# Performance work log

Hardware: AMD Instinct MI355X
Metric: run time of the kernel (lower is better)

The kernel has to match this reference:

```python
import jax, jax.numpy as jnp
import numpy as np

H = 64  # latent_dim // 2


def _lstm_cell(x, h, c, Wih, Whh, b):
    # PyTorch gate order: i, f, g, o
    g = x @ Wih.T + h @ Whh.T + b
    i, f, gg, o = jnp.split(g, 4, axis=-1)
    c = jax.nn.sigmoid(f) * c + jax.nn.sigmoid(i) * jnp.tanh(gg)
    h = jax.nn.sigmoid(o) * jnp.tanh(c)
    return h, c


def _run_lstm(x, Wih, Whh, b):
    # x: [B, T, D] -> outputs [B, T, H], final h, c (zero-initialized state)
    B = x.shape[0]
    h0 = jnp.zeros((B, Whh.shape[1]), x.dtype)

    def step(carry, xt):
        h, c = _lstm_cell(xt, carry[0], carry[1], Wih, Whh, b)
        return (h, c), h

    (h, c), ys = jax.lax.scan(step, (h0, h0), jnp.swapaxes(x, 0, 1))
    return jnp.swapaxes(ys, 0, 1), h, c


def setup_inputs() -> dict:
    key = jax.random.key(0)
    ks = jax.random.split(key, 16)
    B, S, T, D = 512, 1024, 512, 3
    s = 1.0 / np.sqrt(H)

    def u(k, shape):
        return jax.random.uniform(k, shape, jnp.float32, -s, s)

    return {
        "src": jax.random.normal(ks[0], (B, S, D), jnp.float32),
        "trg": jax.random.normal(ks[1], (B, T, D), jnp.float32),
        "enc1_Wih": u(ks[2], (4 * H, D)),
        "enc1_Whh": u(ks[3], (4 * H, H)),
        "enc1_b": u(ks[4], (4 * H,)),
        "enc2_Wih": u(ks[5], (4 * H, H)),
        "enc2_Whh": u(ks[6], (4 * H, H)),
        "enc2_b": u(ks[7], (4 * H,)),
        "dec1_Wih": u(ks[8], (4 * H, D)),
        "dec1_Whh": u(ks[9], (4 * H, H)),
        "dec1_b": u(ks[10], (4 * H,)),
        "dec2_Wih": u(ks[11], (4 * H, H)),
        "dec2_Whh": u(ks[12], (4 * H, H)),
        "dec2_b": u(ks[13], (4 * H,)),
        "fc_W": u(ks[14], (D, H)),
        "fc_b": u(ks[15], (D,)),
    }


def reference(src, trg, enc1_Wih, enc1_Whh, enc1_b, enc2_Wih, enc2_Whh, enc2_b,
              dec1_Wih, dec1_Whh, dec1_b, dec2_Wih, dec2_Whh, dec2_b, fc_W, fc_b):
    # Encoder: two stacked LSTMs over src; keep final state of layer 2.
    y1, _, _ = _run_lstm(src, enc1_Wih, enc1_Whh, enc1_b)
    _, h, c = _run_lstm(y1, enc2_Wih, enc2_Whh, enc2_b)

    # Decoder (teacher_forcing_ratio = 1.0, the only well-defined branch):
    # at each step both decoder LSTMs share/chain the SAME (h, c) state,
    # exactly as the original Decoder.forward does with seq-len-1 inputs.
    def step(carry, xt):
        h, c = carry
        h1, c1 = _lstm_cell(xt, h, c, dec1_Wih, dec1_Whh, dec1_b)
        h2, c2 = _lstm_cell(h1, h1, c1, dec2_Wih, dec2_Whh, dec2_b)
        return (h2, c2), h2 @ fc_W.T + fc_b

    xs = jnp.swapaxes(trg[:, :-1, :], 0, 1)  # inputs for t = 1..T-1
    _, preds = jax.lax.scan(step, (h, c), xs)
    preds = jnp.swapaxes(preds, 0, 1)  # [B, T-1, 3]

    B = trg.shape[0]
    zero0 = jnp.zeros((B, 1, fc_b.shape[0]), preds.dtype)  # outputs[:, 0] stays 0
    return jnp.concatenate([zero0, preds], axis=1)
```

## Files before the change

### kernel.cpp

```cpp
#include <hip/hip_runtime.h>
#include <math.h>

typedef _Float16 f16;
typedef _Float16 f16x8 __attribute__((ext_vector_type(8)));
typedef float    f32x4 __attribute__((ext_vector_type(4)));

#define MFMA16(A, B, C) __builtin_amdgcn_mfma_f32_16x16x32_f16((A), (B), (C), 0, 0, 0)
#define LOG2E 1.44269504088896f

__device__ __forceinline__ float sig2(float a) {
    return __builtin_amdgcn_rcpf(1.0f + __builtin_amdgcn_exp2f(a));
}
__device__ __forceinline__ float tanh2(float c) {
    return fmaf(2.0f, sig2(c * (-2.0f * LOG2E)), -1.0f);
}

__device__ __forceinline__ f16x8 ldfrag(const float* __restrict__ W, int n, int k0, float s) {
    const float* p = W + (size_t)n * 64 + k0;
    f16x8 r;
#pragma unroll
    for (int j = 0; j < 8; j++) r[j] = (f16)(s * p[j]);
    return r;
}

__global__ __launch_bounds__(512, 2)
void seq2seq_kernel(const float* __restrict__ src, const float* __restrict__ trg,
                    const float* __restrict__ e1ih, const float* __restrict__ e1hh,
                    const float* __restrict__ e1b,
                    const float* __restrict__ e2ih, const float* __restrict__ e2hh,
                    const float* __restrict__ e2b,
                    const float* __restrict__ d1ih, const float* __restrict__ d1hh,
                    const float* __restrict__ d1b,
                    const float* __restrict__ d2ih, const float* __restrict__ d2hh,
                    const float* __restrict__ d2b,
                    const float* __restrict__ fcW, const float* __restrict__ fcb,
                    float* __restrict__ out)
{
    const int bp   = blockIdx.x;
    const int tid  = threadIdx.x;
    const int wv   = tid >> 6;
    const bool isB = (wv >= 4);
    const int wvg  = wv & 3;
    const int lane = tid & 63;
    const int quad = lane >> 4;
    const int c15  = lane & 15;
    const int u16  = wvg * 16 + c15;
    const int qb   = quad & 1;
    const int ab   = c15 & 1;

    __shared__ __align__(16) float xst[1024][8];
    __shared__ __align__(16) float tst[512][8];
    __shared__ __align__(16) f16 h1l[2][2][64];
    __shared__ __align__(16) f16 h2l[2][2][64];
    __shared__ float c1buf[2][64];
    __shared__ float c2buf[2][64];
    __shared__ __align__(16) f16 ring[2][16][72];

    {
        const float* s0 = src + (size_t)(2 * bp) * 3072;
        const float* s1 = s0 + 3072;
        for (int i = tid; i < 3072; i += 512) {
            int t = i / 3, c = i - 3 * t;
            xst[t][c]     = s0[i];
            xst[t][4 + c] = s1[i];
        }
        const float* t0p = trg + (size_t)(2 * bp) * 1536;
        const float* t1p = t0p + 1536;
        for (int i = tid; i < 1536; i += 512) {
            int t = i / 3, c = i - 3 * t;
            tst[t][c]     = t0p[i];
            tst[t][4 + c] = t1p[i];
        }
    }

    f16x8 E1hh[4][2];
    f16x8 E2ih[4][2], E2hh[4][2];
    float xw[4][3], bias1[4];
    f32x4 bs2[4];
    if (!isB) {
#pragma unroll
        for (int g = 0; g < 4; g++) {
            const float s = (g == 2) ? (-2.0f * LOG2E) : (-LOG2E);
            const int n = g * 64 + u16;
#pragma unroll
            for (int c = 0; c < 2; c++)
                E1hh[g][c] = ldfrag(e1hh, n, c * 32 + quad * 8, s);
            xw[g][0] = s * e1ih[n * 3 + 0];
            xw[g][1] = s * e1ih[n * 3 + 1];
            xw[g][2] = s * e1ih[n * 3 + 2];
            bias1[g] = s * e1b[n];
        }
    } else {
#pragma unroll
        for (int g = 0; g < 4; g++) {
            const float s = (g == 2) ? (-2.0f * LOG2E) : (-LOG2E);
            const int n = g * 64 + u16;
#pragma unroll
            for (int c = 0; c < 2; c++) {
                E2ih[g][c] = ldfrag(e2ih, n, c * 32 + quad * 8, s);
                E2hh[g][c] = ldfrag(e2hh, n, c * 32 + quad * 8, s);
            }
            float bv = s * e2b[n];
            bs2[g] = (f32x4){bv, bv, bv, bv};
        }
    }

    float c1 = 0.f, c2 = 0.f;
    if (tid < 256) {
        (&h1l[0][0][0])[tid] = (f16)0.f;
        (&h2l[0][0][0])[tid] = (f16)0.f;
    }
    __syncthreads();

    const f32x4 z4 = {0.f, 0.f, 0.f, 0.f};

    f32x4 xq = z4, xnq = z4;
    if (!isB) xq = *(const f32x4*)&xst[0][qb * 4];

#pragma unroll 1
    for (int tau = 0; tau <= 1024; tau++) {
        const int w = tau & 1;
        if (!isB) {
            if (tau < 1024) {
                const f16* h1p = h1l[w ^ 1][ab];
                f16x8 a0 = *(const f16x8*)(h1p + quad * 8);
                f16x8 a1 = *(const f16x8*)(h1p + 32 + quad * 8);
                float xt[4];
#pragma unroll
                for (int g = 0; g < 4; g++)
                    xt[g] = fmaf(xw[g][0], xq.x,
                            fmaf(xw[g][1], xq.y, fmaf(xw[g][2], xq.z, bias1[g])));
                f32x4 acc[4];
#pragma unroll
                for (int g = 0; g < 4; g++)
                    acc[g] = MFMA16(a1, E1hh[g][1], MFMA16(a0, E1hh[g][0], z4));
                float v[4];
#pragma unroll
                for (int g = 0; g < 4; g++)
                    v[g] = (qb ? acc[g][1] : acc[g][0]) + xt[g];
                float iv = sig2(v[0]), fv = sig2(v[1]);
                float gv = fmaf(2.0f, sig2(v[2]), -1.0f), ov = sig2(v[3]);
                c1 = fv * c1 + iv * gv;
                if (quad < 2) h1l[w][quad][u16] = (f16)(ov * tanh2(c1));
                const int tn = (tau + 1 < 1024) ? tau + 1 : 1023;
                xnq = *(const f32x4*)&xst[tn][qb * 4];
            }
        } else {
            if (tau > 0) {
                const f16* h1p = h1l[w ^ 1][ab];
                const f16* h2p = h2l[w ^ 1][ab];
                f16x8 a0 = *(const f16x8*)(h1p + quad * 8);
                f16x8 a1 = *(const f16x8*)(h1p + 32 + quad * 8);
                f16x8 b0 = *(const f16x8*)(h2p + quad * 8);
                f16x8 b1 = *(const f16x8*)(h2p + 32 + quad * 8);
                f32x4 accA[4], accB[4];
#pragma unroll
                for (int g = 0; g < 4; g++) {
                    accA[g] = MFMA16(a1, E2ih[g][1], MFMA16(a0, E2ih[g][0], bs2[g]));
                    accB[g] = MFMA16(b1, E2hh[g][1], MFMA16(b0, E2hh[g][0], z4));
                }
                float v[4];
#pragma unroll
                for (int g = 0; g < 4; g++)
                    v[g] = (qb ? accA[g][1] : accA[g][0]) +
                           (qb ? accB[g][1] : accB[g][0]);
                float iv = sig2(v[0]), fv = sig2(v[1]);
                float gv = fmaf(2.0f, sig2(v[2]), -1.0f), ov = sig2(v[3]);
                c2 = fv * c2 + iv * gv;
                if (quad < 2) h2l[w][quad][u16] = (f16)(ov * tanh2(c2));
            }
        }
        __syncthreads();
        if (!isB) xq = xnq;
    }

    f16x8 D1hh[4][2];
    f16x8 W2s[4][2];
    float dxw[4][3], db1[4];
    f32x4 db2s[4];
    if (!isB) {
#pragma unroll
        for (int g = 0; g < 4; g++) {
            const float s = (g == 2) ? (-2.0f * LOG2E) : (-LOG2E);
            const int n = g * 64 + u16;
#pragma unroll
            for (int c = 0; c < 2; c++)
                D1hh[g][c] = ldfrag(d1hh, n, c * 32 + quad * 8, s);
            dxw[g][0] = s * d1ih[n * 3 + 0];
            dxw[g][1] = s * d1ih[n * 3 + 1];
            dxw[g][2] = s * d1ih[n * 3 + 2];
            db1[g] = s * d1b[n];
        }
    } else {
#pragma unroll
        for (int g = 0; g < 4; g++) {
            const float s = (g == 2) ? (-2.0f * LOG2E) : (-LOG2E);
            const int n = g * 64 + u16;
#pragma unroll
            for (int c = 0; c < 2; c++) {
                const int k0 = c * 32 + quad * 8;
                const float* pa = d2ih + (size_t)n * 64 + k0;
                const float* pb = d2hh + (size_t)n * 64 + k0;
                f16x8 r;
#pragma unroll
                for (int j = 0; j < 8; j++) r[j] = (f16)(s * (pa[j] + pb[j]));
                W2s[g][c] = r;
            }
            float bv = s * d2b[n];
            db2s[g] = (f32x4){bv, bv, bv, bv};
        }
        if (quad < 2) c2buf[quad][u16] = c2;
    }
    f16x8 FW0 = {}, FW1 = {};
    float fb = 0.f;
    if (wv >= 6 && c15 < 3) {
#pragma unroll
        for (int j = 0; j < 8; j++) {
            FW0[j] = (f16)fcW[c15 * 64 + quad * 8 + j];
            FW1[j] = (f16)fcW[c15 * 64 + 32 + quad * 8 + j];
        }
        fb = fcb[c15];
    }
    __syncthreads();

    f32x4 tq = z4, tnq = z4;
    if (!isB) tq = *(const f32x4*)&tst[0][qb * 4];

#pragma unroll 1
    for (int t = 0; t < 511; t++) {
        const int r = t & 1, w = r ^ 1;
        if (!isB) {
            const f16* hp = h2l[r][ab];
            f16x8 a0 = *(const f16x8*)(hp + quad * 8);
            f16x8 a1 = *(const f16x8*)(hp + 32 + quad * 8);
            float cdin = c2buf[qb][u16];
            float xt[4];
#pragma unroll
            for (int g = 0; g < 4; g++)
                xt[g] = fmaf(dxw[g][0], tq.x,
                        fmaf(dxw[g][1], tq.y, fmaf(dxw[g][2], tq.z, db1[g])));
            f32x4 acc[4];
#pragma unroll
            for (int g = 0; g < 4; g++)
                acc[g] = MFMA16(a1, D1hh[g][1], MFMA16(a0, D1hh[g][0], z4));
            float v[4];
#pragma unroll
            for (int g = 0; g < 4; g++)
                v[g] = (qb ? acc[g][1] : acc[g][0]) + xt[g];
            float iv = sig2(v[0]), fv = sig2(v[1]);
            float gv = fmaf(2.0f, sig2(v[2]), -1.0f), ov = sig2(v[3]);
            float c1d = fv * cdin + iv * gv;
            if (quad < 2) {
                h1l[w][quad][u16] = (f16)(ov * tanh2(c1d));
                c1buf[quad][u16]  = c1d;
            }
            const int tn = (t + 1 < 511) ? t + 1 : 510;
            tnq = *(const f32x4*)&tst[tn][qb * 4];
        } else if (wv >= 6 && t > 0 && (t & 15) == 0) {
            const int bsel = wv - 6;
            const f16* rp = &ring[bsel][0][0];
            f16x8 fa0 = *(const f16x8*)(rp + c15 * 72 + quad * 8);
            f16x8 fa1 = *(const f16x8*)(rp + c15 * 72 + 32 + quad * 8);
            f32x4 acc = MFMA16(fa1, FW1, MFMA16(fa0, FW0, z4));
            if (c15 < 3) {
                float* ob = out + (((size_t)(2 * bp + bsel) * 512 + (t - 15)) * 3) + c15;
#pragma unroll
                for (int rg = 0; rg < 4; rg++)
                    ob[(quad * 4 + rg) * 3] = acc[rg] + fb;
            }
        }
        __syncthreads();
        if (!isB) tq = tnq;

        if (isB) {
            const f16* np = h1l[w][ab];
            f16x8 m0 = *(const f16x8*)(np + quad * 8);
            f16x8 m1 = *(const f16x8*)(np + 32 + quad * 8);
            float c1in = c1buf[qb][u16];
            f32x4 acc[4];
#pragma unroll
            for (int g = 0; g < 4; g++)
                acc[g] = MFMA16(m1, W2s[g][1], MFMA16(m0, W2s[g][0], db2s[g]));
            float v[4];
#pragma unroll
            for (int g = 0; g < 4; g++)
                v[g] = (qb ? acc[g][1] : acc[g][0]);
            float i2 = sig2(v[0]), f2 = sig2(v[1]);
            float g2 = fmaf(2.0f, sig2(v[2]), -1.0f), o2 = sig2(v[3]);
            float c2d = f2 * c1in + i2 * g2;
            if (quad < 2) {
                f16 hh = (f16)(o2 * tanh2(c2d));
                h2l[w][quad][u16] = hh;
                c2buf[quad][u16]  = c2d;
                ring[quad][t & 15][u16] = hh;
            }
        }
        __syncthreads();
    }

    if (wv >= 6) {
        const int bsel = wv - 6;
        const f16* rp = &ring[bsel][0][0];
        f16x8 fa0 = *(const f16x8*)(rp + c15 * 72 + quad * 8);
        f16x8 fa1 = *(const f16x8*)(rp + c15 * 72 + 32 + quad * 8);
        f32x4 acc = MFMA16(fa1, FW1, MFMA16(fa0, FW0, z4));
        if (c15 < 3) {
            float* ob = out + (((size_t)(2 * bp + bsel) * 512 + 497) * 3) + c15;
#pragma unroll
            for (int rg = 0; rg < 4; rg++) {
                int step = quad * 4 + rg;
                if (step < 15) ob[step * 3] = acc[rg] + fb;
            }
        }
    }
}

extern "C" void kernel_launch(void* const* d_in, const int* in_sizes, int n_in,
                              void* d_out, int out_size, void* d_ws, size_t ws_size,
                              hipStream_t stream)
{
    const float* src   = (const float*)d_in[0];
    const float* trg   = (const float*)d_in[1];
    const float* e1ih  = (const float*)d_in[2];
    const float* e1hh  = (const float*)d_in[3];
    const float* e1b   = (const float*)d_in[4];
    const float* e2ih  = (const float*)d_in[5];
    const float* e2hh  = (const float*)d_in[6];
    const float* e2b   = (const float*)d_in[7];
    const float* dd1ih = (const float*)d_in[8];
    const float* dd1hh = (const float*)d_in[9];
    const float* dd1b  = (const float*)d_in[10];
    const float* dd2ih = (const float*)d_in[11];
    const float* dd2hh = (const float*)d_in[12];
    const float* dd2b  = (const float*)d_in[13];
    const float* fcW   = (const float*)d_in[14];
    const float* fcb   = (const float*)d_in[15];
    float* out = (float*)d_out;

    hipMemsetAsync(d_out, 0, (size_t)out_size * sizeof(float), stream);

    seq2seq_kernel<<<256, 512, 0, stream>>>(src, trg,
                                            e1ih, e1hh, e1b, e2ih, e2hh, e2b,
                                            dd1ih, dd1hh, dd1b, dd2ih, dd2hh, dd2b,
                                            fcW, fcb, out);
}
```

Baseline: 832.3 us.

## Split encoder LSTM step into two barrier phases so MFMA overlaps activations

```diff
diff --git a/kernel.cpp b/kernel.cpp
--- a/kernel.cpp
+++ b/kernel.cpp
@@ -114,64 +114,84 @@
 
     const f32x4 z4 = {0.f, 0.f, 0.f, 0.f};
 
-    f32x4 xq = z4, xnq = z4;
+    f32x4 xq = z4;
     if (!isB) xq = *(const f32x4*)&xst[0][qb * 4];
+
+    f32x4 accA[4], accB[4];
 
 #pragma unroll 1
     for (int tau = 0; tau <= 1024; tau++) {
-        const int w = tau & 1;
+        const int w = tau & 1, r = w ^ 1;
+
         if (!isB) {
             if (tau < 1024) {
-                const f16* h1p = h1l[w ^ 1][ab];
+                const f16* h1p = h1l[r][ab];
                 f16x8 a0 = *(const f16x8*)(h1p + quad * 8);
                 f16x8 a1 = *(const f16x8*)(h1p + 32 + quad * 8);
+                __builtin_amdgcn_s_setprio(1);
+#pragma unroll
+                for (int g = 0; g < 4; g++)
+                    accA[g] = MFMA16(a1, E1hh[g][1], MFMA16(a0, E1hh[g][0], z4));
+                __builtin_amdgcn_s_setprio(0);
+            }
+        } else if (tau >= 2) {
+            float v[4];
+#pragma unroll
+            for (int g = 0; g < 4; g++)
+                v[g] = (qb ? accA[g][1] : accA[g][0]) +
+                       (qb ? accB[g][1] : accB[g][0]);
+            float iv = sig2(v[0]), fv = sig2(v[1]);
+            float gv = fmaf(2.0f, sig2(v[2]), -1.0f), ov = sig2(v[3]);
+            c2 = fv * c2 + iv * gv;
+            if (quad < 2) h2l[w][quad][u16] = (f16)(ov * tanh2(c2));
+        }
+        __syncthreads();
+
+        if (!isB) {
+            if (tau < 1024) {
                 float xt[4];
 #pragma unroll
                 for (int g = 0; g < 4; g++)
                     xt[g] = fmaf(xw[g][0], xq.x,
                             fmaf(xw[g][1], xq.y, fmaf(xw[g][2], xq.z, bias1[g])));
-                f32x4 acc[4];
+                float v[4];
 #pragma unroll
                 for (int g = 0; g < 4; g++)
-                    acc[g] = MFMA16(a1, E1hh[g][1], MFMA16(a0, E1hh[g][0], z4));
-                float v[4];
-#pragma unroll
-                for (int g = 0; g < 4; g++)
-                    v[g] = (qb ? acc[g][1] : acc[g][0]) + xt[g];
+                    v[g] = (qb ? accA[g][1] : accA[g][0]) + xt[g];
                 float iv = sig2(v[0]), fv = sig2(v[1]);
                 float gv = fmaf(2.0f, sig2(v[2]), -1.0f), ov = sig2(v[3]);
                 c1 = fv * c1 + iv * gv;
                 if (quad < 2) h1l[w][quad][u16] = (f16)(ov * tanh2(c1));
                 const int tn = (tau + 1 < 1024) ? tau + 1 : 1023;
-                xnq = *(const f32x4*)&xst[tn][qb * 4];
-            }
-        } else {
-            if (tau > 0) {
-                const f16* h1p = h1l[w ^ 1][ab];
-                const f16* h2p = h2l[w ^ 1][ab];
-                f16x8 a0 = *(const f16x8*)(h1p + quad * 8);
-                f16x8 a1 = *(const f16x8*)(h1p + 32 + quad * 8);
-                f16x8 b0 = *(const f16x8*)(h2p + quad * 8);
-                f16x8 b1 = *(const f16x8*)(h2p + 32 + quad * 8);
-                f32x4 accA[4], accB[4];
-#pragma unroll
-                for (int g = 0; g < 4; g++) {
-                    accA[g] = MFMA16(a1, E2ih[g][1], MFMA16(a0, E2ih[g][0], bs2[g]));
-                    accB[g] = MFMA16(b1, E2hh[g][1], MFMA16(b0, E2hh[g][0], z4));
-                }
-                float v[4];
-#pragma unroll
-                for (int g = 0; g < 4; g++)
-                    v[g] = (qb ? accA[g][1] : accA[g][0]) +
-                           (qb ? accB[g][1] : accB[g][0]);
-                float iv = sig2(v[0]), fv = sig2(v[1]);
-                float gv = fmaf(2.0f, sig2(v[2]), -1.0f), ov = sig2(v[3]);
-                c2 = fv * c2 + iv * gv;
-                if (quad < 2) h2l[w][quad][u16] = (f16)(ov * tanh2(c2));
-            }
+                xq = *(const f32x4*)&xst[tn][qb * 4];
+            }
+        } else if (tau >= 1) {
+            const f16* h1p = h1l[r][ab];
+            const f16* h2p = h2l[w][ab];
+            f16x8 a0 = *(const f16x8*)(h1p + quad * 8);
+            f16x8 a1 = *(const f16x8*)(h1p + 32 + quad * 8);
+            f16x8 b0 = *(const f16x8*)(h2p + quad * 8);
+            f16x8 b1 = *(const f16x8*)(h2p + 32 + quad * 8);
+            __builtin_amdgcn_s_setprio(1);
+#pragma unroll
+            for (int g = 0; g < 4; g++) {
+                accA[g] = MFMA16(a1, E2ih[g][1], MFMA16(a0, E2ih[g][0], bs2[g]));
+                accB[g] = MFMA16(b1, E2hh[g][1], MFMA16(b0, E2hh[g][0], z4));
+            }
+            __builtin_amdgcn_s_setprio(0);
         }
         __syncthreads();
-        if (!isB) xq = xnq;
+    }
+    if (isB) {
+        float v[4];
+#pragma unroll
+        for (int g = 0; g < 4; g++)
+            v[g] = (qb ? accA[g][1] : accA[g][0]) +
+                   (qb ? accB[g][1] : accB[g][0]);
+        float iv = sig2(v[0]), fv = sig2(v[1]);
+        float gv = fmaf(2.0f, sig2(v[2]), -1.0f), ov = sig2(v[3]);
+        c2 = fv * c2 + iv * gv;
+        if (quad < 2) h2l[0][quad][u16] = (f16)(ov * tanh2(c2));
     }
 
     f16x8 D1hh[4][2];
@@ -201,10 +221,10 @@
                 const int k0 = c * 32 + quad * 8;
                 const float* pa = d2ih + (size_t)n * 64 + k0;
                 const float* pb = d2hh + (size_t)n * 64 + k0;
-                f16x8 r;
-#pragma unroll
-                for (int j = 0; j < 8; j++) r[j] = (f16)(s * (pa[j] + pb[j]));
-                W2s[g][c] = r;
+                f16x8 r2;
+#pragma unroll
+                for (int j = 0; j < 8; j++) r2[j] = (f16)(s * (pa[j] + pb[j]));
+                W2s[g][c] = r2;
             }
             float bv = s * d2b[n];
             db2s[g] = (f32x4){bv, bv, bv, bv};
@@ -240,9 +260,11 @@
                 xt[g] = fmaf(dxw[g][0], tq.x,
                         fmaf(dxw[g][1], tq.y, fmaf(dxw[g][2], tq.z, db1[g])));
             f32x4 acc[4];
+            __builtin_amdgcn_s_setprio(1);
 #pragma unroll
             for (int g = 0; g < 4; g++)
                 acc[g] = MFMA16(a1, D1hh[g][1], MFMA16(a0, D1hh[g][0], z4));
+            __builtin_amdgcn_s_setprio(0);
             float v[4];
 #pragma unroll
             for (int g = 0; g < 4; g++)
@@ -278,9 +300,11 @@
             f16x8 m1 = *(const f16x8*)(np + 32 + quad * 8);
             float c1in = c1buf[qb][u16];
             f32x4 acc[4];
+            __builtin_amdgcn_s_setprio(1);
 #pragma unroll
             for (int g = 0; g < 4; g++)
                 acc[g] = MFMA16(m1, W2s[g][1], MFMA16(m0, W2s[g][0], db2s[g]));
+            __builtin_amdgcn_s_setprio(0);
             float v[4];
 #pragma unroll
             for (int g = 0; g < 4; g++)
```

Result: slower. 1.580 ms (+89.9%).

## Replace per-step block barriers with LDS flag handshakes between wave groups

Applied to the files above, without the earlier changes.

```diff
diff --git a/kernel.cpp b/kernel.cpp
--- a/kernel.cpp
+++ b/kernel.cpp
@@ -21,6 +21,31 @@
 #pragma unroll
     for (int j = 0; j < 8; j++) r[j] = (f16)(s * p[j]);
     return r;
+}
+
+__device__ __forceinline__ void poll4(volatile unsigned* f, unsigned want) {
+    int g = 0;
+    for (;;) {
+        unsigned a = f[0], b = f[1], c = f[2], d = f[3];
+        if ((a >= want) & (b >= want) & (c >= want) & (d >= want)) break;
+        if (++g > (1 << 22)) break;
+    }
+    asm volatile("" ::: "memory");
+}
+__device__ __forceinline__ void poll44(volatile unsigned* f, unsigned wa, unsigned wb) {
+    int g = 0;
+    for (;;) {
+        unsigned a = f[0], b = f[1], c = f[2], d = f[3];
+        unsigned e = f[4], h = f[5], i = f[6], j = f[7];
+        if ((a >= wa) & (b >= wa) & (c >= wa) & (d >= wa) &
+            (e >= wb) & (h >= wb) & (i >= wb) & (j >= wb)) break;
+        if (++g > (1 << 22)) break;
+    }
+    asm volatile("" ::: "memory");
+}
+__device__ __forceinline__ void publish(volatile unsigned* f, int idx, unsigned v, bool doit) {
+    asm volatile("s_waitcnt lgkmcnt(0)" ::: "memory");
+    if (doit) f[idx] = v;
 }
 
 __global__ __launch_bounds__(512, 2)
@@ -50,11 +75,14 @@
 
     __shared__ __align__(16) float xst[1024][8];
     __shared__ __align__(16) float tst[512][8];
-    __shared__ __align__(16) f16 h1l[2][2][64];
-    __shared__ __align__(16) f16 h2l[2][2][64];
+    __shared__ __align__(16) f16 h1l[4][2][64];
+    __shared__ __align__(16) f16 h2l[4][2][64];
     __shared__ float c1buf[2][64];
     __shared__ float c2buf[2][64];
     __shared__ __align__(16) f16 ring[2][16][72];
+    __shared__ unsigned flg[16];
+
+    volatile unsigned* vflg = flg;
 
     {
         const float* s0 = src + (size_t)(2 * bp) * 3072;
@@ -106,78 +134,77 @@
     }
 
     float c1 = 0.f, c2 = 0.f;
-    if (tid < 256) {
+    if (tid < 512) {
         (&h1l[0][0][0])[tid] = (f16)0.f;
         (&h2l[0][0][0])[tid] = (f16)0.f;
     }
+    if (tid < 16) flg[tid] = 0;
     __syncthreads();
 
     const f32x4 z4 = {0.f, 0.f, 0.f, 0.f};
 
-    f32x4 xq = z4, xnq = z4;
-    if (!isB) xq = *(const f32x4*)&xst[0][qb * 4];
-
+    if (!isB) {
 #pragma unroll 1
-    for (int tau = 0; tau <= 1024; tau++) {
-        const int w = tau & 1;
-        if (!isB) {
-            if (tau < 1024) {
-                const f16* h1p = h1l[w ^ 1][ab];
-                f16x8 a0 = *(const f16x8*)(h1p + quad * 8);
-                f16x8 a1 = *(const f16x8*)(h1p + 32 + quad * 8);
-                float xt[4];
-#pragma unroll
-                for (int g = 0; g < 4; g++)
-                    xt[g] = fmaf(xw[g][0], xq.x,
-                            fmaf(xw[g][1], xq.y, fmaf(xw[g][2], xq.z, bias1[g])));
-                f32x4 acc[4];
-#pragma unroll
-                for (int g = 0; g < 4; g++)
-                    acc[g] = MFMA16(a1, E1hh[g][1], MFMA16(a0, E1hh[g][0], z4));
-                float v[4];
-#pragma unroll
-                for (int g = 0; g < 4; g++)
-                    v[g] = (qb ? acc[g][1] : acc[g][0]) + xt[g];
-                float iv = sig2(v[0]), fv = sig2(v[1]);
-                float gv = fmaf(2.0f, sig2(v[2]), -1.0f), ov = sig2(v[3]);
-                c1 = fv * c1 + iv * gv;
-                if (quad < 2) h1l[w][quad][u16] = (f16)(ov * tanh2(c1));
-                const int tn = (tau + 1 < 1024) ? tau + 1 : 1023;
-                xnq = *(const f32x4*)&xst[tn][qb * 4];
-            }
-        } else {
-            if (tau > 0) {
-                const f16* h1p = h1l[w ^ 1][ab];
-                const f16* h2p = h2l[w ^ 1][ab];
-                f16x8 a0 = *(const f16x8*)(h1p + quad * 8);
-                f16x8 a1 = *(const f16x8*)(h1p + 32 + quad * 8);
-                f16x8 b0 = *(const f16x8*)(h2p + quad * 8);
-                f16x8 b1 = *(const f16x8*)(h2p + 32 + quad * 8);
-                f32x4 accA[4], accB[4];
-#pragma unroll
-                for (int g = 0; g < 4; g++) {
-                    accA[g] = MFMA16(a1, E2ih[g][1], MFMA16(a0, E2ih[g][0], bs2[g]));
-                    accB[g] = MFMA16(b1, E2hh[g][1], MFMA16(b0, E2hh[g][0], z4));
-                }
-                float v[4];
-#pragma unroll
-                for (int g = 0; g < 4; g++)
-                    v[g] = (qb ? accA[g][1] : accA[g][0]) +
-                           (qb ? accB[g][1] : accB[g][0]);
-                float iv = sig2(v[0]), fv = sig2(v[1]);
-                float gv = fmaf(2.0f, sig2(v[2]), -1.0f), ov = sig2(v[3]);
-                c2 = fv * c2 + iv * gv;
-                if (quad < 2) h2l[w][quad][u16] = (f16)(ov * tanh2(c2));
-            }
-        }
-        __syncthreads();
-        if (!isB) xq = xnq;
+        for (unsigned tau = 0; tau < 1024; tau++) {
+            f32x4 xq = *(const f32x4*)&xst[tau][qb * 4];
+            poll44(vflg, tau, tau >= 3 ? tau - 3 : 0);
+            const f16* h1p = h1l[(tau + 3) & 3][ab];
+            f16x8 a0 = *(const f16x8*)(h1p + quad * 8);
+            f16x8 a1 = *(const f16x8*)(h1p + 32 + quad * 8);
+            float xt[4];
+#pragma unroll
+            for (int g = 0; g < 4; g++)
+                xt[g] = fmaf(xw[g][0], xq.x,
+                        fmaf(xw[g][1], xq.y, fmaf(xw[g][2], xq.z, bias1[g])));
+            f32x4 acc[4];
+#pragma unroll
+            for (int g = 0; g < 4; g++)
+                acc[g] = MFMA16(a1, E1hh[g][1], MFMA16(a0, E1hh[g][0], z4));
+            float v[4];
+#pragma unroll
+            for (int g = 0; g < 4; g++)
+                v[g] = (qb ? acc[g][1] : acc[g][0]) + xt[g];
+            float iv = sig2(v[0]), fv = sig2(v[1]);
+            float gv = fmaf(2.0f, sig2(v[2]), -1.0f), ov = sig2(v[3]);
+            c1 = fv * c1 + iv * gv;
+            if (quad < 2) h1l[tau & 3][quad][u16] = (f16)(ov * tanh2(c1));
+            publish(vflg, wvg, tau + 1, lane == 0);
+        }
+    } else {
+#pragma unroll 1
+        for (unsigned tau = 1; tau <= 1024; tau++) {
+            poll44(vflg, tau, tau - 1);
+            const f16* h1p = h1l[(tau + 3) & 3][ab];
+            const f16* h2p = h2l[(tau + 2) & 3][ab];
+            f16x8 a0 = *(const f16x8*)(h1p + quad * 8);
+            f16x8 a1 = *(const f16x8*)(h1p + 32 + quad * 8);
+            f16x8 b0 = *(const f16x8*)(h2p + quad * 8);
+            f16x8 b1 = *(const f16x8*)(h2p + 32 + quad * 8);
+            f32x4 accA[4], accB[4];
+#pragma unroll
+            for (int g = 0; g < 4; g++) {
+                accA[g] = MFMA16(a1, E2ih[g][1], MFMA16(a0, E2ih[g][0], bs2[g]));
+                accB[g] = MFMA16(b1, E2hh[g][1], MFMA16(b0, E2hh[g][0], z4));
+            }
+            float v[4];
+#pragma unroll
+            for (int g = 0; g < 4; g++)
+                v[g] = (qb ? accA[g][1] : accA[g][0]) +
+                       (qb ? accB[g][1] : accB[g][0]);
+            float iv = sig2(v[0]), fv = sig2(v[1]);
+            float gv = fmaf(2.0f, sig2(v[2]), -1.0f), ov = sig2(v[3]);
+            c2 = fv * c2 + iv * gv;
+            if (quad < 2) h2l[(tau + 3) & 3][quad][u16] = (f16)(ov * tanh2(c2));
+            publish(vflg + 4, wvg, tau, lane == 0);
+        }
     }
 
     f16x8 D1hh[4][2];
     f16x8 W2s[4][2];
     float dxw[4][3], db1[4];
     f32x4 db2s[4];
+    f16x8 FW0 = {}, FW1 = {};
+    float fb = 0.f;
     if (!isB) {
 #pragma unroll
         for (int g = 0; g < 4; g++) {
@@ -201,36 +228,32 @@
                 const int k0 = c * 32 + quad * 8;
                 const float* pa = d2ih + (size_t)n * 64 + k0;
                 const float* pb = d2hh + (size_t)n * 64 + k0;
-                f16x8 r;
-#pragma unroll
-                for (int j = 0; j < 8; j++) r[j] = (f16)(s * (pa[j] + pb[j]));
-                W2s[g][c] = r;
+                f16x8 r2;
+#pragma unroll
+                for (int j = 0; j < 8; j++) r2[j] = (f16)(s * (pa[j] + pb[j]));
+                W2s[g][c] = r2;
             }
             float bv = s * d2b[n];
             db2s[g] = (f32x4){bv, bv, bv, bv};
         }
         if (quad < 2) c2buf[quad][u16] = c2;
-    }
-    f16x8 FW0 = {}, FW1 = {};
-    float fb = 0.f;
-    if (wv >= 6 && c15 < 3) {
-#pragma unroll
-        for (int j = 0; j < 8; j++) {
-            FW0[j] = (f16)fcW[c15 * 64 + quad * 8 + j];
-            FW1[j] = (f16)fcW[c15 * 64 + 32 + quad * 8 + j];
-        }
-        fb = fcb[c15];
+        if (wv >= 6 && c15 < 3) {
+#pragma unroll
+            for (int j = 0; j < 8; j++) {
+                FW0[j] = (f16)fcW[c15 * 64 + quad * 8 + j];
+                FW1[j] = (f16)fcW[c15 * 64 + 32 + quad * 8 + j];
+            }
+            fb = fcb[c15];
+        }
     }
     __syncthreads();
 
-    f32x4 tq = z4, tnq = z4;
-    if (!isB) tq = *(const f32x4*)&tst[0][qb * 4];
-
+    if (!isB) {
 #pragma unroll 1
-    for (int t = 0; t < 511; t++) {
-        const int r = t & 1, w = r ^ 1;
-        if (!isB) {
-            const f16* hp = h2l[r][ab];
+        for (unsigned t = 0; t < 511; t++) {
+            f32x4 tq = *(const f32x4*)&tst[t][qb * 4];
+            poll4(vflg + 12, t);
+            const f16* hp = h2l[(t + 3) & 3][ab];
             f16x8 a0 = *(const f16x8*)(hp + quad * 8);
             f16x8 a1 = *(const f16x8*)(hp + 32 + quad * 8);
             float cdin = c2buf[qb][u16];
@@ -251,65 +274,66 @@
             float gv = fmaf(2.0f, sig2(v[2]), -1.0f), ov = sig2(v[3]);
             float c1d = fv * cdin + iv * gv;
             if (quad < 2) {
-                h1l[w][quad][u16] = (f16)(ov * tanh2(c1d));
+                h1l[t & 3][quad][u16] = (f16)(ov * tanh2(c1d));
                 c1buf[quad][u16]  = c1d;
             }
-            const int tn = (t + 1 < 511) ? t + 1 : 510;
-            tnq = *(const f32x4*)&tst[tn][qb * 4];
-        } else if (wv >= 6 && t > 0 && (t & 15) == 0) {
+            publish(vflg + 8, wvg, t + 1, lane == 0);
+        }
+    } else {
+#pragma unroll 1
+        for (unsigned t = 0; t < 511; t++) {
+            if (wv >= 6 && t > 0 && (t & 15) == 0) {
+                poll4(vflg + 12, t);
+                const int bsel = wv - 6;
+                const f16* rp = &ring[bsel][0][0];
+                f16x8 fa0 = *(const f16x8*)(rp + c15 * 72 + quad * 8);
+                f16x8 fa1 = *(const f16x8*)(rp + c15 * 72 + 32 + quad * 8);
+                f32x4 acc = MFMA16(fa1, FW1, MFMA16(fa0, FW0, z4));
+                if (c15 < 3) {
+                    float* ob = out + (((size_t)(2 * bp + bsel) * 512 + (t - 15)) * 3) + c15;
+#pragma unroll
+                    for (int rg = 0; rg < 4; rg++)
+                        ob[(quad * 4 + rg) * 3] = acc[rg] + fb;
+                }
+            }
+            poll4(vflg + 8, t + 1);
+            const f16* np = h1l[t & 3][ab];
+            f16x8 m0 = *(const f16x8*)(np + quad * 8);
+            f16x8 m1 = *(const f16x8*)(np + 32 + quad * 8);
+            float c1in = c1buf[qb][u16];
+            f32x4 acc[4];
+#pragma unroll
+            for (int g = 0; g < 4; g++)
+                acc[g] = MFMA16(m1, W2s[g][1], MFMA16(m0, W2s[g][0], db2s[g]));
+            float v[4];
+#pragma unroll
+            for (int g = 0; g < 4; g++)
+                v[g] = (qb ? acc[g][1] : acc[g][0]);
+            float i2 = sig2(v[0]), f2 = sig2(v[1]);
+            float g2 = fmaf(2.0f, sig2(v[2]), -1.0f), o2 = sig2(v[3]);
+            float c2d = f2 * c1in + i2 * g2;
+            if (quad < 2) {
+                f16 hh = (f16)(o2 * tanh2(c2d));
+                h2l[t & 3][quad][u16] = hh;
+                c2buf[quad][u16]  = c2d;
+                ring[quad][t & 15][u16] = hh;
+            }
+            publish(vflg + 12, wvg, t + 1, lane == 0);
+        }
+        if (wv >= 6) {
+            poll4(vflg + 12, 511);
             const int bsel = wv - 6;
             const f16* rp = &ring[bsel][0][0];
             f16x8 fa0 = *(const f16x8*)(rp + c15 * 72 + quad * 8);
             f16x8 fa1 = *(const f16x8*)(rp + c15 * 72 + 32 + quad * 8);
             f32x4 acc = MFMA16(fa1, FW1, MFMA16(fa0, FW0, z4));
             if (c15 < 3) {
-                float* ob = out + (((size_t)(2 * bp + bsel) * 512 + (t - 15)) * 3) + c15;
-#pragma unroll
-                for (int rg = 0; rg < 4; rg++)
-                    ob[(quad * 4 + rg) * 3] = acc[rg] + fb;
-            }
-        }
-        __syncthreads();
-        if (!isB) tq = tnq;
-
-        if (isB) {
-            const f16* np = h1l[w][ab];
-            f16x8 m0 = *(const f16x8*)(np + quad * 8);
-            f16x8 m1 = *(const f16x8*)(np + 32 + quad * 8);
-            float c1in = c1buf[qb][u16];
-            f32x4 acc[4];
-#pragma unroll
-            for (int g = 0; g < 4; g++)
-                acc[g] = MFMA16(m1, W2s[g][1], MFMA16(m0, W2s[g][0], db2s[g]));
-            float v[4];
-#pragma unroll
-            for (int g = 0; g < 4; g++)
-                v[g] = (qb ? acc[g][1] : acc[g][0]);
-            float i2 = sig2(v[0]), f2 = sig2(v[1]);
-            float g2 = fmaf(2.0f, sig2(v[2]), -1.0f), o2 = sig2(v[3]);
-            float c2d = f2 * c1in + i2 * g2;
-            if (quad < 2) {
-                f16 hh = (f16)(o2 * tanh2(c2d));
-                h2l[w][quad][u16] = hh;
-                c2buf[quad][u16]  = c2d;
-                ring[quad][t & 15][u16] = hh;
-            }
-        }
-        __syncthreads();
-    }
-
-    if (wv >= 6) {
-        const int bsel = wv - 6;
-        const f16* rp = &ring[bsel][0][0];
-        f16x8 fa0 = *(const f16x8*)(rp + c15 * 72 + quad * 8);
-        f16x8 fa1 = *(const f16x8*)(rp + c15 * 72 + 32 + quad * 8);
-        f32x4 acc = MFMA16(fa1, FW1, MFMA16(fa0, FW0, z4));
-        if (c15 < 3) {
-            float* ob = out + (((size_t)(2 * bp + bsel) * 512 + 497) * 3) + c15;
-#pragma unroll
-            for (int rg = 0; rg < 4; rg++) {
-                int step = quad * 4 + rg;
-                if (step < 15) ob[step * 3] = acc[rg] + fb;
+                float* ob = out + (((size_t)(2 * bp + bsel) * 512 + 497) * 3) + c15;
+#pragma unroll
+                for (int rg = 0; rg < 4; rg++) {
+                    int step = quad * 4 + rg;
+                    if (step < 15) ob[step * 3] = acc[rg] + fb;
+                }
             }
         }
     }
```

Measured after the change: 1.296 ms. 55.7% more time.

## Pipeline LSTM layers across single wavefronts with LDS flag handoff

Applied to the files above, without the earlier changes.

```diff
diff --git a/kernel.cpp b/kernel.cpp
--- a/kernel.cpp
+++ b/kernel.cpp
@@ -23,7 +23,13 @@
     return r;
 }
 
-__global__ __launch_bounds__(512, 2)
+__device__ __forceinline__ void pollge(volatile unsigned* f, unsigned want) {
+    int g = 0;
+    while (*f < want) { if (++g > (1 << 23)) break; }
+    asm volatile("" ::: "memory");
+}
+
+__global__ __launch_bounds__(256, 1)
 void seq2seq_kernel(const float* __restrict__ src, const float* __restrict__ trg,
                     const float* __restrict__ e1ih, const float* __restrict__ e1hh,
                     const float* __restrict__ e1b,
@@ -39,277 +45,307 @@
     const int bp   = blockIdx.x;
     const int tid  = threadIdx.x;
     const int wv   = tid >> 6;
-    const bool isB = (wv >= 4);
-    const int wvg  = wv & 3;
     const int lane = tid & 63;
     const int quad = lane >> 4;
     const int c15  = lane & 15;
-    const int u16  = wvg * 16 + c15;
     const int qb   = quad & 1;
     const int ab   = c15 & 1;
 
-    __shared__ __align__(16) float xst[1024][8];
-    __shared__ __align__(16) float tst[512][8];
-    __shared__ __align__(16) f16 h1l[2][2][64];
-    __shared__ __align__(16) f16 h2l[2][2][64];
-    __shared__ float c1buf[2][64];
+    __shared__ __align__(16) f16 xst[1024][8];
+    __shared__ __align__(16) f16 tst[512][8];
+    __shared__ __align__(16) f16 h1r[16][2][64];
+    __shared__ __align__(16) f16 h2b[2][64];
+    __shared__ __align__(16) f16 h1d[2][64];
     __shared__ float c2buf[2][64];
-    __shared__ __align__(16) f16 ring[2][16][72];
+    __shared__ __align__(16) f16 ring[2][32][72];
+    __shared__ unsigned flg[4];
+    volatile unsigned* vflg = flg;
 
     {
         const float* s0 = src + (size_t)(2 * bp) * 3072;
         const float* s1 = s0 + 3072;
-        for (int i = tid; i < 3072; i += 512) {
+        for (int i = tid; i < 3072; i += 256) {
             int t = i / 3, c = i - 3 * t;
-            xst[t][c]     = s0[i];
-            xst[t][4 + c] = s1[i];
+            xst[t][c]     = (f16)s0[i];
+            xst[t][4 + c] = (f16)s1[i];
         }
         const float* t0p = trg + (size_t)(2 * bp) * 1536;
         const float* t1p = t0p + 1536;
-        for (int i = tid; i < 1536; i += 512) {
+        for (int i = tid; i < 1536; i += 256) {
             int t = i / 3, c = i - 3 * t;
-            tst[t][c]     = t0p[i];
-            tst[t][4 + c] = t1p[i];
+            tst[t][c]     = (f16)t0p[i];
+            tst[t][4 + c] = (f16)t1p[i];
         }
     }
-
-    f16x8 E1hh[4][2];
-    f16x8 E2ih[4][2], E2hh[4][2];
-    float xw[4][3], bias1[4];
-    f32x4 bs2[4];
-    if (!isB) {
-#pragma unroll
-        for (int g = 0; g < 4; g++) {
+    { f16* z = &h1r[0][0][0]; for (int i = tid; i < 2048; i += 256) z[i] = (f16)0.f; }
+    if (tid < 128) (&h2b[0][0])[tid] = (f16)0.f;
+    if (tid < 4) flg[tid] = 0;
+    __syncthreads();
+
+    const f32x4 z4 = {0.f, 0.f, 0.f, 0.f};
+
+    if (wv == 0) {
+        f16x8 W0[16], W1f[16], XW[16];
+#pragma unroll
+        for (int t = 0; t < 16; t++) {
+            const int g = t >> 2;
             const float s = (g == 2) ? (-2.0f * LOG2E) : (-LOG2E);
-            const int n = g * 64 + u16;
-#pragma unroll
-            for (int c = 0; c < 2; c++)
-                E1hh[g][c] = ldfrag(e1hh, n, c * 32 + quad * 8, s);
-            xw[g][0] = s * e1ih[n * 3 + 0];
-            xw[g][1] = s * e1ih[n * 3 + 1];
-            xw[g][2] = s * e1ih[n * 3 + 2];
-            bias1[g] = s * e1b[n];
+            const int n = g * 64 + (t & 3) * 16 + c15;
+            W0[t]  = ldfrag(e1hh, n, quad * 8, s);
+            W1f[t] = ldfrag(e1hh, n, 32 + quad * 8, s);
+            f16x8 r = {};
+            if (quad == 0) {
+                r[0] = (f16)(s * e1ih[n * 3 + 0]);
+                r[1] = (f16)(s * e1ih[n * 3 + 1]);
+                r[2] = (f16)(s * e1ih[n * 3 + 2]);
+                r[3] = (f16)(s * e1b[n]);
+            }
+            XW[t] = r;
+        }
+        float c1[4] = {0.f, 0.f, 0.f, 0.f};
+#pragma unroll 1
+        for (unsigned tau = 0; tau < 1024; ++tau) {
+            f16x8 xa = {};
+            {
+                const f16* xp = &xst[tau][ab * 4];
+                if (quad == 0) { xa[0] = xp[0]; xa[1] = xp[1]; xa[2] = xp[2]; xa[3] = (f16)1.0f; }
+            }
+            if (tau >= 16 && (tau & 7) == 0) pollge(vflg + 1, tau - 8);
+            f32x4 acc[16];
+#pragma unroll
+            for (int t = 0; t < 16; t++) acc[t] = MFMA16(xa, XW[t], z4);
+            const f16* hb = &h1r[(tau + 15) & 15][0][0];
+            f16x8 a0 = *(const f16x8*)(hb + ab * 64 + quad * 8);
+            f16x8 a1 = *(const f16x8*)(hb + ab * 64 + 32 + quad * 8);
+#pragma unroll
+            for (int t = 0; t < 16; t++)
+                acc[t] = MFMA16(a1, W1f[t], MFMA16(a0, W0[t], acc[t]));
+            float v[16];
+#pragma unroll
+            for (int t = 0; t < 16; t++) v[t] = qb ? acc[t][1] : acc[t][0];
+            f16* hw = &h1r[tau & 15][0][0];
+#pragma unroll
+            for (int ut = 0; ut < 4; ut++) {
+                float iv = sig2(v[ut]), fv = sig2(v[4 + ut]);
+                float gv = fmaf(2.0f, sig2(v[8 + ut]), -1.0f), ov = sig2(v[12 + ut]);
+                c1[ut] = fv * c1[ut] + iv * gv;
+                if (quad < 2) hw[qb * 64 + ut * 16 + c15] = (f16)(ov * tanh2(c1[ut]));
+            }
+            asm volatile("s_waitcnt lgkmcnt(0)" ::: "memory");
+            if (lane == 0) vflg[0] = tau + 1;
+        }
+    } else if (wv == 1) {
+        f16x8 Wi0[16], Wi1[16], Wh0[16], Wh1[16];
+        float b2v[16];
+#pragma unroll
+        for (int t = 0; t < 16; t++) {
+            const int g = t >> 2;
+            const float s = (g == 2) ? (-2.0f * LOG2E) : (-LOG2E);
+            const int n = g * 64 + (t & 3) * 16 + c15;
+            Wi0[t] = ldfrag(e2ih, n, quad * 8, s);
+            Wi1[t] = ldfrag(e2ih, n, 32 + quad * 8, s);
+            Wh0[t] = ldfrag(e2hh, n, quad * 8, s);
+            Wh1[t] = ldfrag(e2hh, n, 32 + quad * 8, s);
+            b2v[t] = s * e2b[n];
+        }
+        float c2r[4] = {0.f, 0.f, 0.f, 0.f};
+#pragma unroll 1
+        for (unsigned tau = 0; tau < 1024; ++tau) {
+            if ((tau & 3) == 0) pollge(vflg + 0, tau + 4);
+            const f16* hb = &h1r[tau & 15][0][0];
+            f16x8 a0 = *(const f16x8*)(hb + ab * 64 + quad * 8);
+            f16x8 a1 = *(const f16x8*)(hb + ab * 64 + 32 + quad * 8);
+            const f16* pb = &h2b[0][0];
+            f16x8 b0 = *(const f16x8*)(pb + ab * 64 + quad * 8);
+            f16x8 b1 = *(const f16x8*)(pb + ab * 64 + 32 + quad * 8);
+            float v[16];
+#pragma unroll
+            for (int h = 0; h < 2; h++) {
+                f32x4 acc[8];
+#pragma unroll
+                for (int tt = 0; tt < 8; tt++) {
+                    const int t = h * 8 + tt;
+                    acc[tt] = MFMA16(b1, Wh1[t], MFMA16(b0, Wh0[t],
+                              MFMA16(a1, Wi1[t], MFMA16(a0, Wi0[t], z4))));
+                }
+#pragma unroll
+                for (int tt = 0; tt < 8; tt++) {
+                    const int t = h * 8 + tt;
+                    v[t] = (qb ? acc[tt][1] : acc[tt][0]) + b2v[t];
+                }
+            }
+            f16* hw = &h2b[0][0];
+#pragma unroll
+            for (int ut = 0; ut < 4; ut++) {
+                float iv = sig2(v[ut]), fv = sig2(v[4 + ut]);
+                float gv = fmaf(2.0f, sig2(v[8 + ut]), -1.0f), ov = sig2(v[12 + ut]);
+                c2r[ut] = fv * c2r[ut] + iv * gv;
+                if (quad < 2) hw[qb * 64 + ut * 16 + c15] = (f16)(ov * tanh2(c2r[ut]));
+            }
+            asm volatile("s_waitcnt lgkmcnt(0)" ::: "memory");
+            if (lane == 0) vflg[1] = tau + 1;
+        }
+#pragma unroll
+        for (int ut = 0; ut < 4; ut++)
+            if (quad < 2) c2buf[qb][ut * 16 + c15] = c2r[ut];
+        asm volatile("s_waitcnt lgkmcnt(0)" ::: "memory");
+        if (lane == 0) vflg[1] = 1026;
+    } else if (wv == 2) {
+        f16x8 D0[16], D1f[16], XW[16], S0[16], S1[16];
+        float b2v[16];
+#pragma unroll
+        for (int t = 0; t < 16; t++) {
+            const int g = t >> 2;
+            const float s = (g == 2) ? (-2.0f * LOG2E) : (-LOG2E);
+            const int n = g * 64 + (t & 3) * 16 + c15;
+            D0[t]  = ldfrag(d1hh, n, quad * 8, s);
+            D1f[t] = ldfrag(d1hh, n, 32 + quad * 8, s);
+            {
+                f16x8 r = {};
+                if (quad == 0) {
+                    r[0] = (f16)(s * d1ih[n * 3 + 0]);
+                    r[1] = (f16)(s * d1ih[n * 3 + 1]);
+                    r[2] = (f16)(s * d1ih[n * 3 + 2]);
+                    r[3] = (f16)(s * d1b[n]);
+                }
+                XW[t] = r;
+            }
+            {
+                const float* pa = d2ih + (size_t)n * 64 + quad * 8;
+                const float* pc = d2hh + (size_t)n * 64 + quad * 8;
+                f16x8 r;
+#pragma unroll
+                for (int j = 0; j < 8; j++) r[j] = (f16)(s * (pa[j] + pc[j]));
+                S0[t] = r;
+            }
+            {
+                const float* pa = d2ih + (size_t)n * 64 + 32 + quad * 8;
+                const float* pc = d2hh + (size_t)n * 64 + 32 + quad * 8;
+                f16x8 r;
+#pragma unroll
+                for (int j = 0; j < 8; j++) r[j] = (f16)(s * (pa[j] + pc[j]));
+                S1[t] = r;
+            }
+            b2v[t] = s * d2b[n];
+        }
+        pollge(vflg + 1, 1026);
+        float c2r[4];
+#pragma unroll
+        for (int ut = 0; ut < 4; ut++) c2r[ut] = c2buf[qb][ut * 16 + c15];
+#pragma unroll 1
+        for (unsigned t = 0; t < 511; ++t) {
+            f16x8 xa = {};
+            {
+                const f16* xp = &tst[t][ab * 4];
+                if (quad == 0) { xa[0] = xp[0]; xa[1] = xp[1]; xa[2] = xp[2]; xa[3] = (f16)1.0f; }
+            }
+            const f16* hb = &h2b[0][0];
+            f16x8 a0 = *(const f16x8*)(hb + ab * 64 + quad * 8);
+            f16x8 a1 = *(const f16x8*)(hb + ab * 64 + 32 + quad * 8);
+            float v[16];
+#pragma unroll
+            for (int h = 0; h < 4; h++) {
+                f32x4 acc[4];
+#pragma unroll
+                for (int tt = 0; tt < 4; tt++) {
+                    const int t2 = h * 4 + tt;
+                    acc[tt] = MFMA16(a1, D1f[t2], MFMA16(a0, D0[t2], MFMA16(xa, XW[t2], z4)));
+                }
+#pragma unroll
+                for (int tt = 0; tt < 4; tt++) {
+                    const int t2 = h * 4 + tt;
+                    v[t2] = qb ? acc[tt][1] : acc[tt][0];
+                }
+            }
+            float c1d[4];
+            f16* hw = &h1d[0][0];
+#pragma unroll
+            for (int ut = 0; ut < 4; ut++) {
+                float iv = sig2(v[ut]), fv = sig2(v[4 + ut]);
+                float gv = fmaf(2.0f, sig2(v[8 + ut]), -1.0f), ov = sig2(v[12 + ut]);
+                c1d[ut] = fv * c2r[ut] + iv * gv;
+                if (quad < 2) hw[qb * 64 + ut * 16 + c15] = (f16)(ov * tanh2(c1d[ut]));
+            }
+            asm volatile("s_waitcnt lgkmcnt(0)" ::: "memory");
+            const f16* np = &h1d[0][0];
+            f16x8 m0 = *(const f16x8*)(np + ab * 64 + quad * 8);
+            f16x8 m1 = *(const f16x8*)(np + ab * 64 + 32 + quad * 8);
+#pragma unroll
+            for (int h = 0; h < 4; h++) {
+                f32x4 acc[4];
+#pragma unroll
+                for (int tt = 0; tt < 4; tt++) {
+                    const int t2 = h * 4 + tt;
+                    acc[tt] = MFMA16(m1, S1[t2], MFMA16(m0, S0[t2], z4));
+                }
+#pragma unroll
+                for (int tt = 0; tt < 4; tt++) {
+                    const int t2 = h * 4 + tt;
+                    v[t2] = (qb ? acc[tt][1] : acc[tt][0]) + b2v[t2];
+                }
+            }
+            f16* hw2 = &h2b[0][0];
+            f16* rw  = &ring[0][0][0];
+#pragma unroll
+            for (int ut = 0; ut < 4; ut++) {
+                float iv = sig2(v[ut]), fv = sig2(v[4 + ut]);
+                float gv = fmaf(2.0f, sig2(v[8 + ut]), -1.0f), ov = sig2(v[12 + ut]);
+                c2r[ut] = fv * c1d[ut] + iv * gv;
+                if (quad < 2) {
+                    f16 hh = (f16)(ov * tanh2(c2r[ut]));
+                    hw2[qb * 64 + ut * 16 + c15] = hh;
+                    rw[qb * 32 * 72 + (t & 31) * 72 + ut * 16 + c15] = hh;
+                }
+            }
+            asm volatile("s_waitcnt lgkmcnt(0)" ::: "memory");
+            if (lane == 0) vflg[2] = t + 1;
         }
     } else {
-#pragma unroll
-        for (int g = 0; g < 4; g++) {
-            const float s = (g == 2) ? (-2.0f * LOG2E) : (-LOG2E);
-            const int n = g * 64 + u16;
-#pragma unroll
-            for (int c = 0; c < 2; c++) {
-                E2ih[g][c] = ldfrag(e2ih, n, c * 32 + quad * 8, s);
-                E2hh[g][c] = ldfrag(e2hh, n, c * 32 + quad * 8, s);
-            }
-            float bv = s * e2b[n];
-            bs2[g] = (f32x4){bv, bv, bv, bv};
-        }
-    }
-
-    float c1 = 0.f, c2 = 0.f;
-    if (tid < 256) {
-        (&h1l[0][0][0])[tid] = (f16)0.f;
-        (&h2l[0][0][0])[tid] = (f16)0.f;
-    }
-    __syncthreads();
-
-    const f32x4 z4 = {0.f, 0.f, 0.f, 0.f};
-
-    f32x4 xq = z4, xnq = z4;
-    if (!isB) xq = *(const f32x4*)&xst[0][qb * 4];
-
+        f16x8 FW0 = {}, FW1 = {};
+        float fb = 0.f;
+        if (c15 < 3) {
+#pragma unroll
+            for (int j = 0; j < 8; j++) {
+                FW0[j] = (f16)fcW[c15 * 64 + quad * 8 + j];
+                FW1[j] = (f16)fcW[c15 * 64 + 32 + quad * 8 + j];
+            }
+            fb = fcb[c15];
+        }
 #pragma unroll 1
-    for (int tau = 0; tau <= 1024; tau++) {
-        const int w = tau & 1;
-        if (!isB) {
-            if (tau < 1024) {
-                const f16* h1p = h1l[w ^ 1][ab];
-                f16x8 a0 = *(const f16x8*)(h1p + quad * 8);
-                f16x8 a1 = *(const f16x8*)(h1p + 32 + quad * 8);
-                float xt[4];
-#pragma unroll
-                for (int g = 0; g < 4; g++)
-                    xt[g] = fmaf(xw[g][0], xq.x,
-                            fmaf(xw[g][1], xq.y, fmaf(xw[g][2], xq.z, bias1[g])));
-                f32x4 acc[4];
-#pragma unroll
-                for (int g = 0; g < 4; g++)
-                    acc[g] = MFMA16(a1, E1hh[g][1], MFMA16(a0, E1hh[g][0], z4));
-                float v[4];
-#pragma unroll
-                for (int g = 0; g < 4; g++)
-                    v[g] = (qb ? acc[g][1] : acc[g][0]) + xt[g];
-                float iv = sig2(v[0]), fv = sig2(v[1]);
-                float gv = fmaf(2.0f, sig2(v[2]), -1.0f), ov = sig2(v[3]);
-                c1 = fv * c1 + iv * gv;
-                if (quad < 2) h1l[w][quad][u16] = (f16)(ov * tanh2(c1));
-                const int tn = (tau + 1 < 1024) ? tau + 1 : 1023;
-                xnq = *(const f32x4*)&xst[tn][qb * 4];
-            }
-        } else {
-            if (tau > 0) {
-                const f16* h1p = h1l[w ^ 1][ab];
-                const f16* h2p = h2l[w ^ 1][ab];
-                f16x8 a0 = *(const f16x8*)(h1p + quad * 8);
-                f16x8 a1 = *(const f16x8*)(h1p + 32 + quad * 8);
-                f16x8 b0 = *(const f16x8*)(h2p + quad * 8);
-                f16x8 b1 = *(const f16x8*)(h2p + 32 + quad * 8);
-                f32x4 accA[4], accB[4];
-#pragma unroll
-                for (int g = 0; g < 4; g++) {
-                    accA[g] = MFMA16(a1, E2ih[g][1], MFMA16(a0, E2ih[g][0], bs2[g]));
-                    accB[g] = MFMA16(b1, E2hh[g][1], MFMA16(b0, E2hh[g][0], z4));
-                }
-                float v[4];
-#pragma unroll
-                for (int g = 0; g < 4; g++)
-                    v[g] = (qb ? accA[g][1] : accA[g][0]) +
-                           (qb ? accB[g][1] : accB[g][0]);
-                float iv = sig2(v[0]), fv = sig2(v[1]);
-                float gv = fmaf(2.0f, sig2(v[2]), -1.0f), ov = sig2(v[3]);
-                c2 = fv * c2 + iv * gv;
-                if (quad < 2) h2l[w][quad][u16] = (f16)(ov * tanh2(c2));
-            }
-        }
-        __syncthreads();
-        if (!isB) xq = xnq;
-    }
-
-    f16x8 D1hh[4][2];
-    f16x8 W2s[4][2];
-    float dxw[4][3], db1[4];
-    f32x4 db2s[4];
-    if (!isB) {
-#pragma unroll
-        for (int g = 0; g < 4; g++) {
-            const float s = (g == 2) ? (-2.0f * LOG2E) : (-LOG2E);
-            const int n = g * 64 + u16;
-#pragma unroll
-            for (int c = 0; c < 2; c++)
-                D1hh[g][c] = ldfrag(d1hh, n, c * 32 + quad * 8, s);
-            dxw[g][0] = s * d1ih[n * 3 + 0];
-            dxw[g][1] = s * d1ih[n * 3 + 1];
-            dxw[g][2] = s * d1ih[n * 3 + 2];
-            db1[g] = s * d1b[n];
-        }
-    } else {
-#pragma unroll
-        for (int g = 0; g < 4; g++) {
-            const float s = (g == 2) ? (-2.0f * LOG2E) : (-LOG2E);
-            const int n = g * 64 + u16;
-#pragma unroll
-            for (int c = 0; c < 2; c++) {
-                const int k0 = c * 32 + quad * 8;
-                const float* pa = d2ih + (size_t)n * 64 + k0;
-                const float* pb = d2hh + (size_t)n * 64 + k0;
-                f16x8 r;
-#pragma unroll
-                for (int j = 0; j < 8; j++) r[j] = (f16)(s * (pa[j] + pb[j]));
-                W2s[g][c] = r;
-            }
-            float bv = s * d2b[n];
-            db2s[g] = (f32x4){bv, bv, bv, bv};
-        }
-        if (quad < 2) c2buf[quad][u16] = c2;
-    }
-    f16x8 FW0 = {}, FW1 = {};
-    float fb = 0.f;
-    if (wv >= 6 && c15 < 3) {
-#pragma unroll
-        for (int j = 0; j < 8; j++) {
-            FW0[j] = (f16)fcW[c15 * 64 + quad * 8 + j];
-            FW1[j] = (f16)fcW[c15 * 64 + 32 + quad * 8 + j];
-        }
-        fb = fcb[c15];
-    }
-    __syncthreads();
-
-    f32x4 tq = z4, tnq = z4;
-    if (!isB) tq = *(const f32x4*)&tst[0][qb * 4];
-
-#pragma unroll 1
-    for (int t = 0; t < 511; t++) {
-        const int r = t & 1, w = r ^ 1;
-        if (!isB) {
-            const f16* hp = h2l[r][ab];
-            f16x8 a0 = *(const f16x8*)(hp + quad * 8);
-            f16x8 a1 = *(const f16x8*)(hp + 32 + quad * 8);
-            float cdin = c2buf[qb][u16];
-            float xt[4];
-#pragma unroll
-            for (int g = 0; g < 4; g++)
-                xt[g] = fmaf(dxw[g][0], tq.x,
-                        fmaf(dxw[g][1], tq.y, fmaf(dxw[g][2], tq.z, db1[g])));
-            f32x4 acc[4];
-#pragma unroll
-            for (int g = 0; g < 4; g++)
-                acc[g] = MFMA16(a1, D1hh[g][1], MFMA16(a0, D1hh[g][0], z4));
-            float v[4];
-#pragma unroll
-            for (int g = 0; g < 4; g++)
-                v[g] = (qb ? acc[g][1] : acc[g][0]) + xt[g];
-            float iv = sig2(v[0]), fv = sig2(v[1]);
-            float gv = fmaf(2.0f, sig2(v[2]), -1.0f), ov = sig2(v[3]);
-            float c1d = fv * cdin + iv * gv;
-            if (quad < 2) {
-                h1l[w][quad][u16] = (f16)(ov * tanh2(c1d));
-                c1buf[quad][u16]  = c1d;
-            }
-            const int tn = (t + 1 < 511) ? t + 1 : 510;
-            tnq = *(const f32x4*)&tst[tn][qb * 4];
-        } else if (wv >= 6 && t > 0 && (t & 15) == 0) {
-            const int bsel = wv - 6;
-            const f16* rp = &ring[bsel][0][0];
-            f16x8 fa0 = *(const f16x8*)(rp + c15 * 72 + quad * 8);
-            f16x8 fa1 = *(const f16x8*)(rp + c15 * 72 + 32 + quad * 8);
-            f32x4 acc = MFMA16(fa1, FW1, MFMA16(fa0, FW0, z4));
-            if (c15 < 3) {
-                float* ob = out + (((size_t)(2 * bp + bsel) * 512 + (t - 15)) * 3) + c15;
-#pragma unroll
-                for (int rg = 0; rg < 4; rg++)
-                    ob[(quad * 4 + rg) * 3] = acc[rg] + fb;
-            }
-        }
-        __syncthreads();
-        if (!isB) tq = tnq;
-
-        if (isB) {
-            const f16* np = h1l[w][ab];
-            f16x8 m0 = *(const f16x8*)(np + quad * 8);
-            f16x8 m1 = *(const f16x8*)(np + 32 + quad * 8);
-            float c1in = c1buf[qb][u16];
-            f32x4 acc[4];
-#pragma unroll
-            for (int g = 0; g < 4; g++)
-                acc[g] = MFMA16(m1, W2s[g][1], MFMA16(m0, W2s[g][0], db2s[g]));
-            float v[4];
-#pragma unroll
-            for (int g = 0; g < 4; g++)
-                v[g] = (qb ? acc[g][1] : acc[g][0]);
-            float i2 = sig2(v[0]), f2 = sig2(v[1]);
-            float g2 = fmaf(2.0f, sig2(v[2]), -1.0f), o2 = sig2(v[3]);
-            float c2d = f2 * c1in + i2 * g2;
-            if (quad < 2) {
-                f16 hh = (f16)(o2 * tanh2(c2d));
-                h2l[w][quad][u16] = hh;
-                c2buf[quad][u16]  = c2d;
-                ring[quad][t & 15][u16] = hh;
-            }
-        }
-        __syncthreads();
-    }
-
-    if (wv >= 6) {
-        const int bsel = wv - 6;
-        const f16* rp = &ring[bsel][0][0];
-        f16x8 fa0 = *(const f16x8*)(rp + c15 * 72 + quad * 8);
-        f16x8 fa1 = *(const f16x8*)(rp + c15 * 72 + 32 + quad * 8);
-        f32x4 acc = MFMA16(fa1, FW1, MFMA16(fa0, FW0, z4));
-        if (c15 < 3) {
-            float* ob = out + (((size_t)(2 * bp + bsel) * 512 + 497) * 3) + c15;
-#pragma unroll
-            for (int rg = 0; rg < 4; rg++) {
-                int step = quad * 4 + rg;
-                if (step < 15) ob[step * 3] = acc[rg] + fb;
+        for (int k = 1; k <= 31; k++) {
+            pollge(vflg + 2, (unsigned)(k * 16));
+            const int base = ((k - 1) * 16) & 31;
+#pragma unroll
+            for (int b = 0; b < 2; b++) {
+                const f16* rp = &ring[b][0][0];
+                f16x8 fa0 = *(const f16x8*)(rp + (base + c15) * 72 + quad * 8);
+                f16x8 fa1 = *(const f16x8*)(rp + (base + c15) * 72 + 32 + quad * 8);
+                f32x4 acc = MFMA16(fa1, FW1, MFMA16(fa0, FW0, z4));
+                if (c15 < 3) {
+                    float* ob = out + (((size_t)(2 * bp + b) * 512 + (k * 16 - 15)) * 3) + c15;
+#pragma unroll
+                    for (int rg = 0; rg < 4; rg++)
+                        ob[(quad * 4 + rg) * 3] = acc[rg] + fb;
+                }
+            }
+        }
+        pollge(vflg + 2, 511);
+        {
+            const int base = 16;
+#pragma unroll
+            for (int b = 0; b < 2; b++) {
+                const f16* rp = &ring[b][0][0];
+                f16x8 fa0 = *(const f16x8*)(rp + (base + c15) * 72 + quad * 8);
+                f16x8 fa1 = *(const f16x8*)(rp + (base + c15) * 72 + 32 + quad * 8);
+                f32x4 acc = MFMA16(fa1, FW1, MFMA16(fa0, FW0, z4));
+                if (c15 < 3) {
+                    float* ob = out + (((size_t)(2 * bp + b) * 512 + 497) * 3) + c15;
+#pragma unroll
+                    for (int rg = 0; rg < 4; rg++) {
+                        int step = quad * 4 + rg;
+                        if (step < 15) ob[step * 3] = acc[rg] + fb;
+                    }
+                }
             }
         }
     }
@@ -339,7 +375,7 @@
 
     hipMemsetAsync(d_out, 0, (size_t)out_size * sizeof(float), stream);
 
-    seq2seq_kernel<<<256, 512, 0, stream>>>(src, trg,
+    seq2seq_kernel<<<256, 256, 0, stream>>>(src, trg,
                                             e1ih, e1hh, e1b, e2ih, e2hh, e2b,
                                             dd1ih, dd1hh, dd1b, dd2ih, dd2hh, dd2b,
                                             fcW, fcb, out);
```

Measured after the change: 2.178 ms. 162% more time.
